# Performance work log

Hardware: AMD Instinct MI355X
Metric: run time of the kernel (lower is better)

Reference implementation:

```python
import jax, jax.numpy as jnp
import numpy as np
from jax import lax

KERNEL = 3
SIGMA = 1.0


def _pdf_gaussian(img):
    # img: [1, 1, H, W]. torch nn.Unfold(k=3, p=1) with zero padding ->
    # patches [1, k*k, H, W] (SAME zero padding), matching torch's [B, L, k*k] after swapaxes.
    patches = lax.conv_general_dilated_patches(
        img, filter_shape=(KERNEL, KERNEL), window_strides=(1, 1), padding='SAME'
    )  # [1, 9, H, W]
    n = KERNEL * KERNEL
    neigh = patches.reshape(1, n, -1).transpose(0, 2, 1)      # [1, HW, 9]
    center = img.reshape(1, -1, 1)                             # [1, HW, 1]
    diff2 = (neigh - center) ** 2
    gauss = jnp.exp(-diff2 / (2.0 * SIGMA * SIGMA))            # [1, HW, 9]
    gauss = gauss / gauss.sum(axis=2, keepdims=True)           # normalize per pixel
    return gauss[0]                                            # [HW, 9]


def setup_inputs() -> dict:
    key = jax.random.key(0)
    k1, k2 = jax.random.split(key)
    H = W = 2048
    pred_real = jax.random.uniform(k1, (1, 1, H, W), dtype=jnp.float32)
    pred_fake = jax.random.uniform(k2, (1, 1, H, W), dtype=jnp.float32)
    return {"pred_real": pred_real, "pred_fake": pred_fake}


def reference(pred_real, pred_fake):
    p = _pdf_gaussian(pred_real)   # [HW, 9]
    q = _pdf_gaussian(pred_fake)   # [HW, 9]
    m = 0.5 * (p + q)
    kl_pq = (p * jnp.log(p / m)).sum(axis=1)   # sum over 9 neighbors
    kl_qp = (q * jnp.log(q / m)).sum(axis=1)
    div = 0.5 * kl_pq + 0.5 * kl_qp            # per-pixel JS divergence
    return 2.0 * div.sum()
```

## Files before the change

### kernel.cpp

```cpp
#include <hip/hip_runtime.h>

static constexpr int H = 2048;
static constexpr int W = 2048;
static constexpr int BLOCK = 256;
static constexpr int PXT = 2;
static constexpr int NBLOCKS = H * (W / (BLOCK * PXT));
static constexpr int RBLOCK = 1024;

__device__ __forceinline__ float fexp2(float x){ return __builtin_amdgcn_exp2f(x); }
__device__ __forceinline__ float flog2(float x){ return __builtin_amdgcn_logf(x); }
__device__ __forceinline__ float frcp (float x){ return __builtin_amdgcn_rcpf(x); }

static constexpr float S_   = 0.84932180028801905f;
static constexpr float LN2_ = 0.69314718055994531f;

__device__ __forceinline__ float pixel_term(
    float aul, float auc, float aur, float adl, float adc, float adr, float ca,
    float heAl, float heAr, float htAl, float htAr,
    float bul, float buc, float bur, float bdl, float bdc, float bdr, float cb,
    float heBl, float heBr, float htBl, float htBr)
{
    float Gp = 1.f + heAl + heAr;
    float Sp = htAl + htAr;
    float Gq = 1.f + heBl + heBr;
    float Sq = htBl + htBr;

    float d, t, e;
#define NB(nv, cv, G, Ssum, ev)                                   \
    d = (nv) - (cv); d *= S_; t = d * d; e = fexp2(-t);           \
    G += e; Ssum = fmaf(e, t, Ssum); const float ev = e;

    NB(aul, ca, Gp, Sp, veA0)  NB(auc, ca, Gp, Sp, veA1)  NB(aur, ca, Gp, Sp, veA2)
    NB(adl, ca, Gp, Sp, veA3)  NB(adc, ca, Gp, Sp, veA4)  NB(adr, ca, Gp, Sp, veA5)
    NB(bul, cb, Gq, Sq, veB0)  NB(buc, cb, Gq, Sq, veB1)  NB(bur, cb, Gq, Sq, veB2)
    NB(bdl, cb, Gq, Sq, veB3)  NB(bdc, cb, Gq, Sq, veB4)  NB(bdr, cb, Gq, Sq, veB5)
#undef NB

    const float ip = frcp(Gp), iq = frcp(Gq);
    const float hp = 0.5f * ip, hq = 0.5f * iq;

    float m = hp + hq;
    float mll = m * flog2(m);
#define MT(ea, eb)                                                \
    m = fmaf((ea), hp, (eb) * hq); mll = fmaf(m, flog2(m), mll);
    MT(heAl, heBl)  MT(heAr, heBr)
    MT(veA0, veB0)  MT(veA1, veB1)  MT(veA2, veB2)
    MT(veA3, veB3)  MT(veA4, veB4)  MT(veA5, veB5)
#undef MT

    return fmaf(Sp, ip, Sq * iq) + flog2(Gp * Gq) + 2.f * mll;
}

__global__ __launch_bounds__(BLOCK, 6) void jsd_pixel_kernel(
    const float* __restrict__ A, const float* __restrict__ B,
    float* __restrict__ partial)
{
    const int bid  = blockIdx.x;
    const int y    = bid >> 2;
    const int x0   = ((bid & 3) << 9) + (threadIdx.x << 1);
    const int base = y * W + x0;
    const bool hasL = (x0 > 0);
    const bool hasR = (x0 + PXT < W);

#define LOAD_ROW(p0,p1,p2,p3, ptr, off)                           \
    { const float2 q_ = *(const float2*)((ptr) + (off));          \
      p1 = q_.x; p2 = q_.y;                                       \
      p0 = hasL ? (ptr)[(off) - 1]   : 0.f;                       \
      p3 = hasR ? (ptr)[(off) + PXT] : 0.f; }

    float a10,a11,a12,a13, b10,b11,b12,b13;
    float a00,a01,a02,a03, b00,b01,b02,b03;
    float a20,a21,a22,a23, b20,b21,b22,b23;

    LOAD_ROW(a10,a11,a12,a13, A, base)
    LOAD_ROW(b10,b11,b12,b13, B, base)
    if (y > 0) {
        LOAD_ROW(a00,a01,a02,a03, A, base - W)
        LOAD_ROW(b00,b01,b02,b03, B, base - W)
    } else {
        a00=a01=a02=a03=0.f; b00=b01=b02=b03=0.f;
    }
    if (y < H - 1) {
        LOAD_ROW(a20,a21,a22,a23, A, base + W)
        LOAD_ROW(b20,b21,b22,b23, B, base + W)
    } else {
        a20=a21=a22=a23=0.f; b20=b21=b22=b23=0.f;
    }
#undef LOAD_ROW

#define HP(he, ht, l, r)                                          \
    float he, ht;                                                 \
    { float d_ = (r) - (l); d_ *= S_; const float t_ = d_ * d_;   \
      he = fexp2(-t_); ht = he * t_; }
    HP(heA0, htA0, a10, a11)  HP(heA1, htA1, a11, a12)  HP(heA2, htA2, a12, a13)
    HP(heB0, htB0, b10, b11)  HP(heB1, htB1, b11, b12)  HP(heB2, htB2, b12, b13)
#undef HP

    float pacc;
    pacc  = pixel_term(a00,a01,a02, a20,a21,a22, a11, heA0,heA1, htA0,htA1,
                       b00,b01,b02, b20,b21,b22, b11, heB0,heB1, htB0,htB1);
    pacc += pixel_term(a01,a02,a03, a21,a22,a23, a12, heA1,heA2, htA1,htA2,
                       b01,b02,b03, b21,b22,b23, b12, heB1,heB2, htB1,htB2);

    #pragma unroll
    for (int off = 32; off > 0; off >>= 1)
        pacc += __shfl_down(pacc, off, 64);

    __shared__ float wsum[BLOCK / 64];
    const int lane = threadIdx.x & 63;
    const int wid  = threadIdx.x >> 6;
    if (lane == 0) wsum[wid] = pacc;
    __syncthreads();
    if (threadIdx.x == 0)
        partial[blockIdx.x] = wsum[0] + wsum[1] + wsum[2] + wsum[3];
}

__global__ __launch_bounds__(RBLOCK) void jsd_final_reduce(
    const float* __restrict__ partial, float* __restrict__ out)
{
    float s = 0.f;
    #pragma unroll
    for (int i = 0; i < NBLOCKS / RBLOCK; ++i)
        s += partial[i * RBLOCK + threadIdx.x];

    #pragma unroll
    for (int off = 32; off > 0; off >>= 1)
        s += __shfl_down(s, off, 64);

    __shared__ float wsum[RBLOCK / 64];
    const int lane = threadIdx.x & 63;
    const int wid  = threadIdx.x >> 6;
    if (lane == 0) wsum[wid] = s;
    __syncthreads();
    if (threadIdx.x == 0) {
        float t = 0.f;
        #pragma unroll
        for (int i = 0; i < RBLOCK / 64; ++i) t += wsum[i];
        out[0] = -LN2_ * t;
    }
}

extern "C" void kernel_launch(void* const* d_in, const int* in_sizes, int n_in,
                              void* d_out, int out_size, void* d_ws, size_t ws_size,
                              hipStream_t stream) {
    const float* A = (const float*)d_in[0];
    const float* B = (const float*)d_in[1];
    float* out = (float*)d_out;
    float* partial = (float*)d_ws;

    jsd_pixel_kernel<<<NBLOCKS, BLOCK, 0, stream>>>(A, B, partial);
    jsd_final_reduce<<<1, RBLOCK, 0, stream>>>(partial, out);
}
```

Baseline: 28.58 us.

## Process 2x2 pixel tile per thread, sharing symmetric pair exponentials across rows

Each thread now computes a 2x2 block of pixels instead of 1x2, loading four rows and evaluating the Gaussian weight of every adjacent pair (horizontal, vertical, diagonal) once and reusing it for both pixels that share the pair. This removes redundant exp2 evaluations and the overlapping halo loads of the old one-row layout, and halves the block count. It also replaces two reciprocals with one reciprocal of the product Gp*Gq. The costs are many more live registers (occupancy hint lowered from 6 to 4 blocks per CU) and fewer blocks in flight.

```diff
diff --git a/kernel.cpp b/kernel.cpp
--- a/kernel.cpp
+++ b/kernel.cpp
@@ -3,8 +3,7 @@
 static constexpr int H = 2048;
 static constexpr int W = 2048;
 static constexpr int BLOCK = 256;
-static constexpr int PXT = 2;
-static constexpr int NBLOCKS = H * (W / (BLOCK * PXT));
+static constexpr int NBLOCKS = (H / 2) * (W / (BLOCK * 2));
 static constexpr int RBLOCK = 1024;
 
 __device__ __forceinline__ float fexp2(float x){ return __builtin_amdgcn_exp2f(x); }
@@ -15,92 +14,107 @@
 static constexpr float LN2_ = 0.69314718055994531f;
 
 __device__ __forceinline__ float pixel_term(
-    float aul, float auc, float aur, float adl, float adc, float adr, float ca,
-    float heAl, float heAr, float htAl, float htAr,
-    float bul, float buc, float bur, float bdl, float bdc, float bdr, float cb,
-    float heBl, float heBr, float htBl, float htBr)
+    float an0, float an1, float an2, float ca,
+    float hAe0, float hAt0, float hAe1, float hAt1,
+    float vAe0, float vAt0, float vAe1, float vAt1, float vAe2, float vAt2,
+    float bn0, float bn1, float bn2, float cb,
+    float hBe0, float hBt0, float hBe1, float hBt1,
+    float vBe0, float vBt0, float vBe1, float vBt1, float vBe2, float vBt2)
 {
-    float Gp = 1.f + heAl + heAr;
-    float Sp = htAl + htAr;
-    float Gq = 1.f + heBl + heBr;
-    float Sq = htBl + htBr;
+    float d, t;
+    d = an0 - ca; d *= S_; t = d*d; const float iAe0 = fexp2(-t); const float iAt0 = iAe0*t;
+    d = an1 - ca; d *= S_; t = d*d; const float iAe1 = fexp2(-t); const float iAt1 = iAe1*t;
+    d = an2 - ca; d *= S_; t = d*d; const float iAe2 = fexp2(-t); const float iAt2 = iAe2*t;
+    d = bn0 - cb; d *= S_; t = d*d; const float iBe0 = fexp2(-t); const float iBt0 = iBe0*t;
+    d = bn1 - cb; d *= S_; t = d*d; const float iBe1 = fexp2(-t); const float iBt1 = iBe1*t;
+    d = bn2 - cb; d *= S_; t = d*d; const float iBe2 = fexp2(-t); const float iBt2 = iBe2*t;
 
-    float d, t, e;
-#define NB(nv, cv, G, Ssum, ev)                                   \
-    d = (nv) - (cv); d *= S_; t = d * d; e = fexp2(-t);           \
-    G += e; Ssum = fmaf(e, t, Ssum); const float ev = e;
+    const float Gp = 1.f + hAe0 + hAe1 + vAe0 + vAe1 + vAe2 + iAe0 + iAe1 + iAe2;
+    const float Sp =       hAt0 + hAt1 + vAt0 + vAt1 + vAt2 + iAt0 + iAt1 + iAt2;
+    const float Gq = 1.f + hBe0 + hBe1 + vBe0 + vBe1 + vBe2 + iBe0 + iBe1 + iBe2;
+    const float Sq =       hBt0 + hBt1 + vBt0 + vBt1 + vBt2 + iBt0 + iBt1 + iBt2;
 
-    NB(aul, ca, Gp, Sp, veA0)  NB(auc, ca, Gp, Sp, veA1)  NB(aur, ca, Gp, Sp, veA2)
-    NB(adl, ca, Gp, Sp, veA3)  NB(adc, ca, Gp, Sp, veA4)  NB(adr, ca, Gp, Sp, veA5)
-    NB(bul, cb, Gq, Sq, veB0)  NB(buc, cb, Gq, Sq, veB1)  NB(bur, cb, Gq, Sq, veB2)
-    NB(bdl, cb, Gq, Sq, veB3)  NB(bdc, cb, Gq, Sq, veB4)  NB(bdr, cb, Gq, Sq, veB5)
-#undef NB
-
-    const float ip = frcp(Gp), iq = frcp(Gq);
+    const float P  = Gp * Gq;
+    const float rP = frcp(P);
+    const float ip = rP * Gq;
+    const float iq = rP * Gp;
     const float hp = 0.5f * ip, hq = 0.5f * iq;
 
     float m = hp + hq;
     float mll = m * flog2(m);
-#define MT(ea, eb)                                                \
-    m = fmaf((ea), hp, (eb) * hq); mll = fmaf(m, flog2(m), mll);
-    MT(heAl, heBl)  MT(heAr, heBr)
-    MT(veA0, veB0)  MT(veA1, veB1)  MT(veA2, veB2)
-    MT(veA3, veB3)  MT(veA4, veB4)  MT(veA5, veB5)
+#define MT(ea, eb) m = fmaf((ea), hp, (eb)*hq); mll = fmaf(m, flog2(m), mll);
+    MT(hAe0, hBe0) MT(hAe1, hBe1)
+    MT(vAe0, vBe0) MT(vAe1, vBe1) MT(vAe2, vBe2)
+    MT(iAe0, iBe0) MT(iAe1, iBe1) MT(iAe2, iBe2)
 #undef MT
 
-    return fmaf(Sp, ip, Sq * iq) + flog2(Gp * Gq) + 2.f * mll;
+    return fmaf(Sp, ip, Sq*iq) + flog2(P) + 2.f*mll;
 }
 
-__global__ __launch_bounds__(BLOCK, 6) void jsd_pixel_kernel(
+__global__ __launch_bounds__(BLOCK, 4) void jsd_pixel_kernel(
     const float* __restrict__ A, const float* __restrict__ B,
     float* __restrict__ partial)
 {
-    const int bid  = blockIdx.x;
-    const int y    = bid >> 2;
-    const int x0   = ((bid & 3) << 9) + (threadIdx.x << 1);
-    const int base = y * W + x0;
+    const int bid   = blockIdx.x;
+    const int ytile = bid >> 2;
+    const int y0    = ytile << 1;
+    const int x0    = ((bid & 3) << 9) + (threadIdx.x << 1);
+    const int base  = y0 * W + x0;
     const bool hasL = (x0 > 0);
-    const bool hasR = (x0 + PXT < W);
+    const bool hasR = (x0 + 2 < W);
 
-#define LOAD_ROW(p0,p1,p2,p3, ptr, off)                           \
-    { const float2 q_ = *(const float2*)((ptr) + (off));          \
-      p1 = q_.x; p2 = q_.y;                                       \
-      p0 = hasL ? (ptr)[(off) - 1]   : 0.f;                       \
-      p3 = hasR ? (ptr)[(off) + PXT] : 0.f; }
+    float a00,a01,a02,a03, a10,a11,a12,a13, a20,a21,a22,a23, a30,a31,a32,a33;
+    float b00,b01,b02,b03, b10,b11,b12,b13, b20,b21,b22,b23, b30,b31,b32,b33;
 
-    float a10,a11,a12,a13, b10,b11,b12,b13;
-    float a00,a01,a02,a03, b00,b01,b02,b03;
-    float a20,a21,a22,a23, b20,b21,b22,b23;
+#define LOAD_ROW(p0,p1,p2,p3, ptr, off) \
+    { const float2 q_ = *(const float2*)((ptr)+(off)); p1=q_.x; p2=q_.y; \
+      p0 = hasL ? (ptr)[(off)-1] : 0.f; p3 = hasR ? (ptr)[(off)+2] : 0.f; }
 
     LOAD_ROW(a10,a11,a12,a13, A, base)
+    LOAD_ROW(a20,a21,a22,a23, A, base + W)
     LOAD_ROW(b10,b11,b12,b13, B, base)
-    if (y > 0) {
+    LOAD_ROW(b20,b21,b22,b23, B, base + W)
+    if (y0 > 0) {
         LOAD_ROW(a00,a01,a02,a03, A, base - W)
         LOAD_ROW(b00,b01,b02,b03, B, base - W)
-    } else {
-        a00=a01=a02=a03=0.f; b00=b01=b02=b03=0.f;
-    }
-    if (y < H - 1) {
-        LOAD_ROW(a20,a21,a22,a23, A, base + W)
-        LOAD_ROW(b20,b21,b22,b23, B, base + W)
-    } else {
-        a20=a21=a22=a23=0.f; b20=b21=b22=b23=0.f;
-    }
+    } else { a00=a01=a02=a03=0.f; b00=b01=b02=b03=0.f; }
+    if (y0 + 2 < H) {
+        LOAD_ROW(a30,a31,a32,a33, A, base + 2*W)
+        LOAD_ROW(b30,b31,b32,b33, B, base + 2*W)
+    } else { a30=a31=a32=a33=0.f; b30=b31=b32=b33=0.f; }
 #undef LOAD_ROW
 
-#define HP(he, ht, l, r)                                          \
-    float he, ht;                                                 \
-    { float d_ = (r) - (l); d_ *= S_; const float t_ = d_ * d_;   \
-      he = fexp2(-t_); ht = he * t_; }
-    HP(heA0, htA0, a10, a11)  HP(heA1, htA1, a11, a12)  HP(heA2, htA2, a12, a13)
-    HP(heB0, htB0, b10, b11)  HP(heB1, htB1, b11, b12)  HP(heB2, htB2, b12, b13)
-#undef HP
+#define PAIR(e,t, u,v) float e,t; { float d_=(v)-(u); d_*=S_; const float q_=d_*d_; \
+                                    e=fexp2(-q_); t=e*q_; }
+    PAIR(hA10,tA10, a10,a11) PAIR(hA11,tA11, a11,a12) PAIR(hA12,tA12, a12,a13)
+    PAIR(hA20,tA20, a20,a21) PAIR(hA21,tA21, a21,a22) PAIR(hA22,tA22, a22,a23)
+    PAIR(hB10,tB10, b10,b11) PAIR(hB11,tB11, b11,b12) PAIR(hB12,tB12, b12,b13)
+    PAIR(hB20,tB20, b20,b21) PAIR(hB21,tB21, b21,b22) PAIR(hB22,tB22, b22,b23)
+    PAIR(vA10,wA10, a11,a20) PAIR(vA11,wA11, a11,a21) PAIR(vA12,wA12, a11,a22)
+    PAIR(vA21,wA21, a12,a21) PAIR(vA22,wA22, a12,a22) PAIR(vA23,wA23, a12,a23)
+    PAIR(vA01,wA01, a10,a21) PAIR(vA32,wA32, a13,a22)
+    PAIR(vB10,wB10, b11,b20) PAIR(vB11,wB11, b11,b21) PAIR(vB12,wB12, b11,b22)
+    PAIR(vB21,wB21, b12,b21) PAIR(vB22,wB22, b12,b22) PAIR(vB23,wB23, b12,b23)
+    PAIR(vB01,wB01, b10,b21) PAIR(vB32,wB32, b13,b22)
+#undef PAIR
 
     float pacc;
-    pacc  = pixel_term(a00,a01,a02, a20,a21,a22, a11, heA0,heA1, htA0,htA1,
-                       b00,b01,b02, b20,b21,b22, b11, heB0,heB1, htB0,htB1);
-    pacc += pixel_term(a01,a02,a03, a21,a22,a23, a12, heA1,heA2, htA1,htA2,
-                       b01,b02,b03, b21,b22,b23, b12, heB1,heB2, htB1,htB2);
+    pacc  = pixel_term(a00,a01,a02, a11, hA10,tA10, hA11,tA11,
+                       vA10,wA10, vA11,wA11, vA12,wA12,
+                       b00,b01,b02, b11, hB10,tB10, hB11,tB11,
+                       vB10,wB10, vB11,wB11, vB12,wB12);
+    pacc += pixel_term(a01,a02,a03, a12, hA11,tA11, hA12,tA12,
+                       vA21,wA21, vA22,wA22, vA23,wA23,
+                       b01,b02,b03, b12, hB11,tB11, hB12,tB12,
+                       vB21,wB21, vB22,wB22, vB23,wB23);
+    pacc += pixel_term(a30,a31,a32, a21, hA20,tA20, hA21,tA21,
+                       vA01,wA01, vA11,wA11, vA21,wA21,
+                       b30,b31,b32, b21, hB20,tB20, hB21,tB21,
+                       vB01,wB01, vB11,wB11, vB21,wB21);
+    pacc += pixel_term(a31,a32,a33, a22, hA21,tA21, hA22,tA22,
+                       vA12,wA12, vA22,wA22, vA32,wA32,
+                       b31,b32,b33, b22, hB21,tB21, hB22,tB22,
+                       vB12,wB12, vB22,wB22, vB32,wB32);
 
     #pragma unroll
     for (int off = 32; off > 0; off >>= 1)
```

Result: faster. 26.78 us, median of 2 (-6.3%).

## Process 2x2 pixel tiles, share vertical/diagonal exps, pack A/B into float2 vectors

Applied to the files above, without the earlier changes.

Each thread now handles a 2x2 pixel block instead of 1x2, so Gaussian weights for pairs between the two rows (vertical and diagonal neighbours) are computed once and reused by both pixels. The A and B images are packed into two-wide vectors to allow packed FP32 math. The two per-image reciprocals are merged into one reciprocal of their product. Unaligned 16-byte loads with clamped offsets plus multiplicative masks replace the branchy halo loads. Occupancy hint drops from 6 to 3 blocks to make room for the higher register use.

```diff
diff --git a/kernel.cpp b/kernel.cpp
--- a/kernel.cpp
+++ b/kernel.cpp
@@ -1,106 +1,103 @@
 #include <hip/hip_runtime.h>
+
+typedef float v2 __attribute__((ext_vector_type(2)));
 
 static constexpr int H = 2048;
 static constexpr int W = 2048;
+static constexpr int NPIX = H * W;
 static constexpr int BLOCK = 256;
-static constexpr int PXT = 2;
-static constexpr int NBLOCKS = H * (W / (BLOCK * PXT));
+static constexpr int NBLOCKS = (H / 2) * (W / (BLOCK * 2));
 static constexpr int RBLOCK = 1024;
 
 __device__ __forceinline__ float fexp2(float x){ return __builtin_amdgcn_exp2f(x); }
 __device__ __forceinline__ float flog2(float x){ return __builtin_amdgcn_logf(x); }
 __device__ __forceinline__ float frcp (float x){ return __builtin_amdgcn_rcpf(x); }
 
-static constexpr float S_   = 0.84932180028801905f;
 static constexpr float LN2_ = 0.69314718055994531f;
+static constexpr float S2_  = 0.72134752044448170f;
+
+struct __align__(4) f4u { float x, y, z, w; };
+
+#define PAIRP(e2, w2, U, V)                                           \
+    v2 e2, w2;                                                        \
+    { const v2 d_ = (V) - (U); const v2 t_ = (d_ * d_) * S2_;         \
+      e2.x = fexp2(-t_.x); e2.y = fexp2(-t_.y); w2 = e2 * t_; }
 
 __device__ __forceinline__ float pixel_term(
-    float aul, float auc, float aur, float adl, float adc, float adr, float ca,
-    float heAl, float heAr, float htAl, float htAr,
-    float bul, float buc, float bur, float bdl, float bdc, float bdr, float cb,
-    float heBl, float heBr, float htBl, float htBr)
+    v2 f0, v2 f1, v2 f2, v2 c,
+    v2 he0, v2 hw0, v2 he1, v2 hw1,
+    v2 ve0, v2 vw0, v2 ve1, v2 vw1, v2 ve2, v2 vw2)
 {
-    float Gp = 1.f + heAl + heAr;
-    float Sp = htAl + htAr;
-    float Gq = 1.f + heBl + heBr;
-    float Sq = htBl + htBr;
+    PAIRP(ie0, iw0, f0, c)  PAIRP(ie1, iw1, f1, c)  PAIRP(ie2, iw2, f2, c)
 
-    float d, t, e;
-#define NB(nv, cv, G, Ssum, ev)                                   \
-    d = (nv) - (cv); d *= S_; t = d * d; e = fexp2(-t);           \
-    G += e; Ssum = fmaf(e, t, Ssum); const float ev = e;
+    const v2 G2 = 1.0f + he0 + he1 + ve0 + ve1 + ve2 + ie0 + ie1 + ie2;
+    const v2 T2 =        hw0 + hw1 + vw0 + vw1 + vw2 + iw0 + iw1 + iw2;
 
-    NB(aul, ca, Gp, Sp, veA0)  NB(auc, ca, Gp, Sp, veA1)  NB(aur, ca, Gp, Sp, veA2)
-    NB(adl, ca, Gp, Sp, veA3)  NB(adc, ca, Gp, Sp, veA4)  NB(adr, ca, Gp, Sp, veA5)
-    NB(bul, cb, Gq, Sq, veB0)  NB(buc, cb, Gq, Sq, veB1)  NB(bur, cb, Gq, Sq, veB2)
-    NB(bdl, cb, Gq, Sq, veB3)  NB(bdc, cb, Gq, Sq, veB4)  NB(bdr, cb, Gq, Sq, veB5)
-#undef NB
+    const float P  = G2.x * G2.y;
+    const float rP = frcp(P);
+    v2 ipq;  ipq.x = rP * G2.y;  ipq.y = rP * G2.x;
+    const v2 hpq = ipq * 0.5f;
 
-    const float ip = frcp(Gp), iq = frcp(Gq);
-    const float hp = 0.5f * ip, hq = 0.5f * iq;
+    const v2 ent2 = T2 * ipq;
+    const float base = ent2.x + ent2.y + flog2(P);
 
-    float m = hp + hq;
+    float m = hpq.x + hpq.y;
     float mll = m * flog2(m);
-#define MT(ea, eb)                                                \
-    m = fmaf((ea), hp, (eb) * hq); mll = fmaf(m, flog2(m), mll);
-    MT(heAl, heBl)  MT(heAr, heBr)
-    MT(veA0, veB0)  MT(veA1, veB1)  MT(veA2, veB2)
-    MT(veA3, veB3)  MT(veA4, veB4)  MT(veA5, veB5)
-#undef MT
+#define MTP(e2) { const v2 t_ = (e2) * hpq; const float m_ = t_.x + t_.y; \
+                  mll = fmaf(m_, flog2(m_), mll); }
+    MTP(he0) MTP(he1) MTP(ve0) MTP(ve1) MTP(ve2) MTP(ie0) MTP(ie1) MTP(ie2)
+#undef MTP
 
-    return fmaf(Sp, ip, Sq * iq) + flog2(Gp * Gq) + 2.f * mll;
+    return fmaf(2.f, mll, base);
 }
 
-__global__ __launch_bounds__(BLOCK, 6) void jsd_pixel_kernel(
+__global__ __launch_bounds__(BLOCK, 3) void jsd_pixel_kernel(
     const float* __restrict__ A, const float* __restrict__ B,
     float* __restrict__ partial)
 {
     const int bid  = blockIdx.x;
-    const int y    = bid >> 2;
+    const int y0   = (bid >> 2) << 1;
     const int x0   = ((bid & 3) << 9) + (threadIdx.x << 1);
-    const int base = y * W + x0;
-    const bool hasL = (x0 > 0);
-    const bool hasR = (x0 + PXT < W);
+    const int base = y0 * W + x0;
+    const float mL = (x0 > 0)     ? 1.f : 0.f;
+    const float mR = (x0 + 2 < W) ? 1.f : 0.f;
 
-#define LOAD_ROW(p0,p1,p2,p3, ptr, off)                           \
-    { const float2 q_ = *(const float2*)((ptr) + (off));          \
-      p1 = q_.x; p2 = q_.y;                                       \
-      p0 = hasL ? (ptr)[(off) - 1]   : 0.f;                       \
-      p3 = hasR ? (ptr)[(off) + PXT] : 0.f; }
+    v2 X00,X01,X02,X03, X10,X11,X12,X13, X20,X21,X22,X23, X30,X31,X32,X33;
 
-    float a10,a11,a12,a13, b10,b11,b12,b13;
-    float a00,a01,a02,a03, b00,b01,b02,b03;
-    float a20,a21,a22,a23, b20,b21,b22,b23;
+#define LOAD_PACK(P0,P1,P2,P3, off)                                     \
+    { const f4u a_ = *(const f4u*)(A + (off));                          \
+      const f4u b_ = *(const f4u*)(B + (off));                          \
+      P0 = v2{a_.x, b_.x}; P1 = v2{a_.y, b_.y};                         \
+      P2 = v2{a_.z, b_.z}; P3 = v2{a_.w, b_.w}; }
 
-    LOAD_ROW(a10,a11,a12,a13, A, base)
-    LOAD_ROW(b10,b11,b12,b13, B, base)
-    if (y > 0) {
-        LOAD_ROW(a00,a01,a02,a03, A, base - W)
-        LOAD_ROW(b00,b01,b02,b03, B, base - W)
-    } else {
-        a00=a01=a02=a03=0.f; b00=b01=b02=b03=0.f;
-    }
-    if (y < H - 1) {
-        LOAD_ROW(a20,a21,a22,a23, A, base + W)
-        LOAD_ROW(b20,b21,b22,b23, B, base + W)
-    } else {
-        a20=a21=a22=a23=0.f; b20=b21=b22=b23=0.f;
-    }
-#undef LOAD_ROW
+    LOAD_PACK(X10,X11,X12,X13, max(base - 1, 0))
+    LOAD_PACK(X20,X21,X22,X23, min(base + W - 1, NPIX - 4))
+    if (y0 > 0) {
+        LOAD_PACK(X00,X01,X02,X03, base - W - 1)
+    } else { X00=v2{0,0}; X01=v2{0,0}; X02=v2{0,0}; X03=v2{0,0}; }
+    if (y0 + 2 < H) {
+        LOAD_PACK(X30,X31,X32,X33, base + 2*W - 1)
+    } else { X30=v2{0,0}; X31=v2{0,0}; X32=v2{0,0}; X33=v2{0,0}; }
+#undef LOAD_PACK
 
-#define HP(he, ht, l, r)                                          \
-    float he, ht;                                                 \
-    { float d_ = (r) - (l); d_ *= S_; const float t_ = d_ * d_;   \
-      he = fexp2(-t_); ht = he * t_; }
-    HP(heA0, htA0, a10, a11)  HP(heA1, htA1, a11, a12)  HP(heA2, htA2, a12, a13)
-    HP(heB0, htB0, b10, b11)  HP(heB1, htB1, b11, b12)  HP(heB2, htB2, b12, b13)
-#undef HP
+    X00 *= mL; X10 *= mL; X20 *= mL; X30 *= mL;
+    X03 *= mR; X13 *= mR; X23 *= mR; X33 *= mR;
+
+    PAIRP(h1e0,h1w0, X10,X11) PAIRP(h1e1,h1w1, X11,X12) PAIRP(h1e2,h1w2, X12,X13)
+    PAIRP(h2e0,h2w0, X20,X21) PAIRP(h2e1,h2w1, X21,X22) PAIRP(h2e2,h2w2, X22,X23)
+    PAIRP(v10e,v10w, X11,X20) PAIRP(v11e,v11w, X11,X21) PAIRP(v12e,v12w, X11,X22)
+    PAIRP(v21e,v21w, X12,X21) PAIRP(v22e,v22w, X12,X22) PAIRP(v23e,v23w, X12,X23)
+    PAIRP(v01e,v01w, X10,X21) PAIRP(v32e,v32w, X13,X22)
 
     float pacc;
-    pacc  = pixel_term(a00,a01,a02, a20,a21,a22, a11, heA0,heA1, htA0,htA1,
-                       b00,b01,b02, b20,b21,b22, b11, heB0,heB1, htB0,htB1);
-    pacc += pixel_term(a01,a02,a03, a21,a22,a23, a12, heA1,heA2, htA1,htA2,
-                       b01,b02,b03, b21,b22,b23, b12, heB1,heB2, htB1,htB2);
+    pacc  = pixel_term(X00,X01,X02, X11, h1e0,h1w0, h1e1,h1w1,
+                       v10e,v10w, v11e,v11w, v12e,v12w);
+    pacc += pixel_term(X01,X02,X03, X12, h1e1,h1w1, h1e2,h1w2,
+                       v21e,v21w, v22e,v22w, v23e,v23w);
+    pacc += pixel_term(X30,X31,X32, X21, h2e0,h2w0, h2e1,h2w1,
+                       v01e,v01w, v11e,v11w, v21e,v21w);
+    pacc += pixel_term(X31,X32,X33, X22, h2e1,h2w1, h2e2,h2w2,
+                       v12e,v12w, v22e,v22w, v32e,v32w);
 
     #pragma unroll
     for (int off = 32; off > 0; off >>= 1)
```

Result: faster. 27.07 us (-5.3%).
